# Kernel optimization log

Measured on AMD Instinct MI355X. Metric: run time of the kernel, lower is better.

The kernel has to match this reference:

```python
import jax, jax.numpy as jnp
import numpy as np

K = 32              # neighbors per node (loop=False in knn_graph)
NEG_SLOPE = 0.2     # GATv2Conv default negative_slope


def setup_inputs() -> dict:
    key = jax.random.key(0)
    ks = jax.random.split(key, 5)
    N, D_IN, D_OUT = 10000, 128, 256
    x = jax.random.normal(ks[0], (N, D_IN), dtype=jnp.float32)
    s_in = 1.0 / np.sqrt(D_IN)
    s_out = 1.0 / np.sqrt(D_OUT)
    return {
        "x": x,
        "W_l": jax.random.normal(ks[1], (D_IN, D_OUT), dtype=jnp.float32) * s_in,
        "b_l": jnp.zeros((D_OUT,), dtype=jnp.float32),
        "W_r": jax.random.normal(ks[2], (D_IN, D_OUT), dtype=jnp.float32) * s_in,
        "b_r": jnp.zeros((D_OUT,), dtype=jnp.float32),
        "att": jax.random.normal(ks[3], (D_OUT,), dtype=jnp.float32) * s_out,
        "bias": jnp.zeros((D_OUT,), dtype=jnp.float32),
    }


def _knn_indices(x, k):
    # Squared euclidean cdist, diagonal masked (loop=False), k smallest per row.
    sq = jnp.sum(x * x, axis=1)                       # [N]
    d = sq[:, None] + sq[None, :] - 2.0 * (x @ x.T)   # [N, N]
    d = d + jnp.diag(jnp.full((x.shape[0],), jnp.inf, dtype=x.dtype))
    _, nbr = jax.lax.top_k(-d, k)                     # [N, k] nearest neighbor ids
    return nbr


def reference(x, W_l, b_l, W_r, b_r, att, bias):
    N = x.shape[0]
    nbr = _knn_indices(x, K)                                   # [N, K]
    # GATv2Conv adds self-loops by default -> each node has K+1 sources.
    src = jnp.concatenate([nbr, jnp.arange(N)[:, None]], axis=1)  # [N, K+1]
    h_l = x @ W_l + b_l                                        # source transform [N, D]
    h_r = x @ W_r + b_r                                        # target transform [N, D]
    z = h_l[src] + h_r[:, None, :]                             # [N, K+1, D]
    e = jnp.einsum('nkd,d->nk', jax.nn.leaky_relu(z, NEG_SLOPE), att)  # [N, K+1]
    alpha = jax.nn.softmax(e, axis=1)                          # softmax over sources per target
    out = jnp.einsum('nk,nkd->nd', alpha, h_l[src]) + bias     # [N, D]
    return out
```

## Files before the change

### kernel.cpp

```cpp
#include <hip/hip_runtime.h>
#include <hip/hip_fp16.h>

#define NN     10000
#define DI     128
#define DO     256
#define KNB    32
#define NSRC   33
#define RB     16
#define NP2    10240
#define NTILE  640
#define ATILE  626
#define NCB    20
#define SEG    64
#define CAP    1024
#define RCAND  128
#define NEG    0.2f

typedef __attribute__((ext_vector_type(8))) short bf16x8;
typedef __attribute__((ext_vector_type(4))) float f32x4;

__device__ __forceinline__ unsigned fkey(float f) {
    unsigned u = __float_as_uint(f);
    return (u & 0x80000000u) ? ~u : (u | 0x80000000u);
}
__device__ __forceinline__ unsigned short bf16rne(float f) {
    unsigned u = __float_as_uint(f);
    unsigned r = u + 0x7FFFu + ((u >> 16) & 1u);
    return (unsigned short)(r >> 16);
}

__global__ __launch_bounds__(256) void prep_k(const float* __restrict__ x,
    unsigned short* __restrict__ Bh, double* __restrict__ sq64,
    float* __restrict__ sq32, unsigned* __restrict__ cnt)
{
    __shared__ float xs[16][132];
    const int t = threadIdx.x;
    const int tile = blockIdx.x;
    const int i0 = tile * 16;
    if (tile < 40) {
        const int idx = tile * 256 + t;
        if (idx < ATILE * 16) cnt[idx] = 0;
    }
#pragma unroll
    for (int q = 0; q < 2; ++q) {
        const int idx = t + 256 * q;
        const int r = idx >> 5, c4 = idx & 31;
        float4 v = make_float4(0.f, 0.f, 0.f, 0.f);
        if (i0 + r < NN) v = *(const float4*)(x + (size_t)(i0 + r) * DI + c4 * 4);
        *(float4*)&xs[r][c4 * 4] = v;
    }
    __syncthreads();
    const int ks = t >> 6, flane = t & 63;
    const int srow = flane & 15;
    const int kb = ks * 32 + ((flane >> 4) & 3) * 8;
    unsigned hi2[4];
#pragma unroll
    for (int j = 0; j < 4; ++j) {
        const float v0 = xs[srow][kb + 2 * j], v1 = xs[srow][kb + 2 * j + 1];
        hi2[j] = (unsigned)bf16rne(v0) | ((unsigned)bf16rne(v1) << 16);
    }
    *(uint4*)(Bh + ((size_t)(tile * 4 + ks) * 64 + flane) * 8) =
        make_uint4(hi2[0], hi2[1], hi2[2], hi2[3]);
    const int row = t >> 4, sub = t & 15;
    double s = 0.0;
#pragma unroll
    for (int q = 0; q < 8; ++q) {
        const float v = xs[row][sub * 8 + q];
        s = fma((double)v, (double)v, s);
    }
#pragma unroll
    for (int off = 8; off >= 1; off >>= 1) s += __shfl_xor(s, off);
    if (sub == 0) {
        const int gi = i0 + row;
        sq32[gi] = (gi < NN) ? (float)s : 0.f;
        if (gi < ATILE * 16) sq64[gi] = s;
    }
}

__global__ __launch_bounds__(256) void thresh_k(
    const unsigned short* __restrict__ Bh, const float* __restrict__ sq32,
    unsigned* __restrict__ Trow)
{
    __shared__ unsigned short dist16[RB][512];
    const int rt = blockIdx.x;
    const int r0 = rt * 16;
    const int t = threadIdx.x;
    const int wid = t >> 6, lane = t & 63;
    const int wbase = wid * 128, l15 = lane & 15, rgrp = (lane >> 4) * 4;

    bf16x8 ah[4];
#pragma unroll
    for (int ks = 0; ks < 4; ++ks)
        ah[ks] = *(const bf16x8*)(Bh + ((size_t)(rt * 4 + ks) * 64 + lane) * 8);
    float sqiv[4];
#pragma unroll
    for (int rg = 0; rg < 4; ++rg) sqiv[rg] = sq32[r0 + rgrp + rg];

#pragma unroll 1
    for (int ct = 0; ct < 8; ++ct) {
        const int ctg = wid * 8 + ct;
        bf16x8 bh[4];
#pragma unroll
        for (int ks = 0; ks < 4; ++ks)
            bh[ks] = *(const bf16x8*)(Bh + ((size_t)(ctg * 4 + ks) * 64 + lane) * 8);
        f32x4 acc = {0.f, 0.f, 0.f, 0.f};
#pragma unroll
        for (int ks = 0; ks < 4; ++ks)
            acc = __builtin_amdgcn_mfma_f32_16x16x32_bf16(ah[ks], bh[ks], acc, 0, 0, 0);
        const int col = wbase + ct * 16 + l15;
        const float sqj = sq32[col];
#pragma unroll
        for (int rg = 0; rg < 4; ++rg) {
            const int row = r0 + rgrp + rg;
            const float dd = __builtin_fmaf(-2.f, acc[rg], sqiv[rg] + sqj);
            unsigned k16 = (__float_as_uint(dd) >> 16) | 0x8000u;
            if (col >= NN || col == row) k16 = 0xFFFFu;
            dist16[rgrp + rg][col] = (unsigned short)k16;
        }
    }
    __syncthreads();

#pragma unroll 1
    for (int rr = 0; rr < 4; ++rr) {
        const int r = wid * 4 + rr;
        unsigned kk[8];
#pragma unroll
        for (int u = 0; u < 8; ++u) kk[u] = dist16[r][lane + 64 * u];
        unsigned lo = 0, hi = 0xFFFFu;
#pragma unroll 1
        for (int it = 0; it < 16; ++it) {
            const unsigned mid = (lo + hi) >> 1;
            int c2 = 0;
#pragma unroll
            for (int u = 0; u < 8; ++u)
                c2 += (int)__popcll(__ballot(kk[u] <= mid));
            if (c2 >= 16) hi = mid; else lo = mid;
        }
        if (lane == 0) Trow[r0 + r] = ((hi & 0x7FFFu) << 16) | 0xFFFFu;
    }
}

__global__ __launch_bounds__(256) void knn_emit_k(
    const unsigned short* __restrict__ Bh, const float* __restrict__ sq32,
    const unsigned* __restrict__ Trow, unsigned* __restrict__ cnt,
    unsigned* __restrict__ cand)
{
    __shared__ unsigned lcnt[32];
    __shared__ unsigned basebuf[32];
    __shared__ unsigned cbuf[32][SEG];
    const int r0 = blockIdx.x * 32;
    const int cbase = blockIdx.y * 512;
    const int t = threadIdx.x;
    const int wid = t >> 6, lane = t & 63;
    const int wbase = wid * 128, l15 = lane & 15, rgrp = (lane >> 4) * 4;
    if (t < 32) lcnt[t] = 0;

    bf16x8 ah[2][4];
#pragma unroll
    for (int rt2 = 0; rt2 < 2; ++rt2)
#pragma unroll
        for (int ks = 0; ks < 4; ++ks) {
            const int rt = (r0 >> 4) + rt2;
            ah[rt2][ks] = *(const bf16x8*)(Bh + ((size_t)(rt * 4 + ks) * 64 + lane) * 8);
        }
    float sqiv[2][4];
    unsigned TUv[2][4];
#pragma unroll
    for (int rt2 = 0; rt2 < 2; ++rt2)
#pragma unroll
        for (int rg = 0; rg < 4; ++rg) {
            const int row = r0 + rt2 * 16 + rgrp + rg;
            sqiv[rt2][rg] = sq32[row];
            TUv[rt2][rg] = Trow[row];
        }
    float sqjv[8];
#pragma unroll
    for (int ct = 0; ct < 8; ++ct)
        sqjv[ct] = sq32[cbase + wbase + ct * 16 + l15];
    __syncthreads();

    const int ctg0 = (cbase >> 4) + wid * 8;
    bf16x8 bh[4];
#pragma unroll
    for (int ks = 0; ks < 4; ++ks)
        bh[ks] = *(const bf16x8*)(Bh + ((size_t)(ctg0 * 4 + ks) * 64 + lane) * 8);

#pragma unroll 1
    for (int ct = 0; ct < 8; ++ct) {
        bf16x8 bhn[4];
        if (ct < 7) {
#pragma unroll
            for (int ks = 0; ks < 4; ++ks)
                bhn[ks] = *(const bf16x8*)(Bh + ((size_t)((ctg0 + ct + 1) * 4 + ks) * 64 + lane) * 8);
        }
        f32x4 a0 = {0.f, 0.f, 0.f, 0.f}, a1 = {0.f, 0.f, 0.f, 0.f};
#pragma unroll
        for (int ks = 0; ks < 4; ++ks) {
            a0 = __builtin_amdgcn_mfma_f32_16x16x32_bf16(ah[0][ks], bh[ks], a0, 0, 0, 0);
            a1 = __builtin_amdgcn_mfma_f32_16x16x32_bf16(ah[1][ks], bh[ks], a1, 0, 0, 0);
        }
        const int col = cbase + wbase + ct * 16 + l15;
        const float sqj = sqjv[ct];
#pragma unroll
        for (int rt2 = 0; rt2 < 2; ++rt2)
#pragma unroll
            for (int rg = 0; rg < 4; ++rg) {
                const int lrow = rt2 * 16 + rgrp + rg;
                const float dd = __builtin_fmaf(-2.f, (rt2 ? a1 : a0)[rg],
                                                sqiv[rt2][rg] + sqj);
                const unsigned raw = __float_as_uint(dd);
                if ((raw <= TUv[rt2][rg]) && (col < NN) && (col != r0 + lrow)) {
                    const unsigned slot = atomicAdd(&lcnt[lrow], 1u);
                    if (slot < SEG)
                        cbuf[lrow][slot] =
                            (((raw >> 16) | 0x8000u) << 16) | (unsigned)col;
                }
            }
#pragma unroll
        for (int ks = 0; ks < 4; ++ks) bh[ks] = bhn[ks];
    }

    __syncthreads();
    if (t < 32) {
        unsigned c = lcnt[t]; if (c > SEG) c = SEG;
        lcnt[t] = c;
        basebuf[t] = atomicAdd(&cnt[r0 + t], c);
    }
    __syncthreads();
#pragma unroll
    for (int q = 0; q < (32 * SEG) / 256; ++q) {
        const int idx = t + 256 * q;
        const int lr = idx >> 6, sl = idx & 63;
        if ((unsigned)sl < lcnt[lr]) {
            const unsigned b = basebuf[lr] + (unsigned)sl;
            if (b < CAP) cand[(size_t)(r0 + lr) * CAP + b] = cbuf[lr][sl];
        }
    }
}

__global__ __launch_bounds__(256) void rerank_select_k(
    const float* __restrict__ x, const double* __restrict__ sq64,
    const unsigned* __restrict__ cand, const unsigned* __restrict__ cnt,
    int* __restrict__ nbr)
{
    __shared__ unsigned hist[256];
    __shared__ unsigned hist2[256];
    __shared__ float xrs[DI];
    __shared__ unsigned cbuf[RCAND];
    __shared__ unsigned long long kbuf[RCAND];
    __shared__ unsigned sel[4];
    const int i = blockIdx.x, t = threadIdx.x;
    const int lane = t & 63;

    hist[t] = 0; hist2[t] = 0;
    if (t < RCAND) cbuf[t] = 0xFFFFFFFFu;
    if (t >= 128 && t < 160)
        *(float4*)&xrs[(t - 128) * 4] =
            *(const float4*)(x + (size_t)i * DI + (t - 128) * 4);
    if (t == 0) { sel[0] = 0xFFFFFFFFu; sel[2] = 0xFFFFu; sel[3] = 0; }
    unsigned n = cnt[i]; if (n > CAP) n = CAP;
    unsigned kk[4];
#pragma unroll
    for (int u = 0; u < 4; ++u) {
        const unsigned idx = (unsigned)t + 256u * u;
        kk[u] = (idx < n) ? cand[(size_t)i * CAP + idx] : 0xFFFFFFFFu;
    }
    __syncthreads();

#pragma unroll
    for (int u = 0; u < 4; ++u)
        if (kk[u] != 0xFFFFFFFFu) atomicAdd(&hist[kk[u] >> 24], 1u);
    __syncthreads();
    if (t < 64) {
        unsigned h[4];
#pragma unroll
        for (int q = 0; q < 4; ++q) h[q] = hist[lane * 4 + q];
        const unsigned s = h[0] + h[1] + h[2] + h[3];
        unsigned pre = s;
#pragma unroll
        for (int off = 1; off < 64; off <<= 1) {
            const unsigned o = __shfl_up(pre, off);
            if (lane >= off) pre += o;
        }
        const unsigned B = pre - s;
        if (B < 64 && B + s >= 64) {
            unsigned c = B, H = 0, rr = 0;
#pragma unroll
            for (int q = 0; q < 4; ++q) {
                if (c < 64 && c + h[q] >= 64) { H = lane * 4 + q; rr = 64 - c; break; }
                c += h[q];
            }
            sel[0] = H; sel[1] = rr;
        }
    }
    __syncthreads();
    const unsigned H = sel[0];

    if (H != 0xFFFFFFFFu) {
#pragma unroll
        for (int u = 0; u < 4; ++u)
            if (kk[u] != 0xFFFFFFFFu && (kk[u] >> 24) == H)
                atomicAdd(&hist2[(kk[u] >> 16) & 0xFFu], 1u);
    }
    __syncthreads();
    if (t < 64 && H != 0xFFFFFFFFu) {
        const unsigned r = sel[1];
        unsigned h[4];
#pragma unroll
        for (int q = 0; q < 4; ++q) h[q] = hist2[lane * 4 + q];
        const unsigned s = h[0] + h[1] + h[2] + h[3];
        unsigned pre = s;
#pragma unroll
        for (int off = 1; off < 64; off <<= 1) {
            const unsigned o = __shfl_up(pre, off);
            if (lane >= off) pre += o;
        }
        const unsigned B = pre - s;
        if (B < r && B + s >= r) {
            unsigned c = B, L = 0;
#pragma unroll
            for (int q = 0; q < 4; ++q) {
                if (c < r && c + h[q] >= r) { L = lane * 4 + q; break; }
                c += h[q];
            }
            sel[2] = (H << 8) | L;
        }
    }
    __syncthreads();
    const unsigned T16 = sel[2];

    {
        const unsigned long long lml = (1ull << lane) - 1;
#pragma unroll
        for (int u = 0; u < 4; ++u) {
            const bool pass = (kk[u] != 0xFFFFFFFFu) && ((kk[u] >> 16) <= T16);
            const unsigned long long b = __ballot(pass);
            unsigned base = 0;
            if (lane == 0 && b) base = atomicAdd(&sel[3], (unsigned)__popcll(b));
            base = __shfl(base, 0);
            if (pass) {
                const int slot = (int)(base + (unsigned)__popcll(b & lml));
                if (slot < RCAND) cbuf[slot] = kk[u];
            }
        }
    }
    __syncthreads();

    const int c = t >> 1, h = t & 1;
    const unsigned cc = cbuf[c];
    const int col = (int)(cc & 0xFFFFu);
    const bool valid = col < NN;
    const float* xc = x + (size_t)(valid ? col : 0) * DI;
    double a = 0.0;
#pragma unroll
    for (int q = 0; q < 16; ++q) {
        const int fi = q * 8 + h * 4;
        const float4 v = *(const float4*)(xc + fi);
        const float4 r4 = *(const float4*)(&xrs[fi]);
        a = fma((double)r4.x, (double)v.x, a);
        a = fma((double)r4.y, (double)v.y, a);
        a = fma((double)r4.z, (double)v.z, a);
        a = fma((double)r4.w, (double)v.w, a);
    }
    a += __shfl_xor(a, 1);
    if (h == 0) {
        unsigned long long key = ~0ull;
        if (valid) {
            const float dd = (float)(sq64[i] + sq64[col] - 2.0 * a);
            key = ((unsigned long long)fkey(dd) << 32) | (unsigned)col;
        }
        kbuf[c] = key;
    }
    __syncthreads();

    if (t < RCAND) {
        const unsigned long long key = kbuf[t];
        int rank = 0;
#pragma unroll 8
        for (int j = 0; j < RCAND; ++j)
            rank += (kbuf[j] < key) ? 1 : 0;
        if (key != ~0ull && rank < KNB)
            nbr[(size_t)i * KNB + rank] = (int)(key & 0xFFFFu);
    }
}

__global__ __launch_bounds__(256) void hgemm_k(
    const float* __restrict__ x, const float* __restrict__ Wl,
    const float* __restrict__ bl, const float* __restrict__ Wr,
    const float* __restrict__ br, __half* __restrict__ hl16, float* __restrict__ hr)
{
    const int c = threadIdx.x;
    const int r0 = blockIdx.x * RB;
    float accl[RB], accr[RB];
    const float blv = bl[c], brv = br[c];
#pragma unroll
    for (int r = 0; r < RB; ++r) { accl[r] = blv; accr[r] = brv; }
    for (int d = 0; d < DI; ++d) {
        const float wl = Wl[d * DO + c];
        const float wr = Wr[d * DO + c];
#pragma unroll
        for (int r = 0; r < RB; ++r) {
            const float xv = x[(size_t)(r0 + r) * DI + d];
            accl[r] = fmaf(xv, wl, accl[r]);
            accr[r] = fmaf(xv, wr, accr[r]);
        }
    }
#pragma unroll
    for (int r = 0; r < RB; ++r) {
        hl16[(size_t)(r0 + r) * DO + c] = __float2half(accl[r]);
        hr[(size_t)(r0 + r) * DO + c] = accr[r];
    }
}

__global__ __launch_bounds__(256) void gat_k(
    const __half* __restrict__ hl16, const float* __restrict__ hr,
    const int* __restrict__ nbr, const float* __restrict__ att,
    const float* __restrict__ bias, float* __restrict__ out)
{
    __shared__ int src[NSRC];
    __shared__ __align__(16) __half hbuf[NSRC][DO];
    __shared__ float eS[NSRC];
    __shared__ float alphaS[NSRC];
    const int i = blockIdx.x, t = threadIdx.x;
    if (t < KNB) src[t] = nbr[(size_t)i * KNB + t];
    if (t == KNB) src[KNB] = i;
    __syncthreads();

    {
        const int sub = t & 31, rb = t >> 5;
#pragma unroll
        for (int s = 0; s < 5; ++s) {
            const int rk = s * 8 + rb;
            if (rk < NSRC)
                *(uint4*)&hbuf[rk][sub * 8] =
                    *(const uint4*)(hl16 + (size_t)src[rk] * DO + sub * 8);
        }
    }
    __syncthreads();

    const int wid = t >> 6, lane = t & 63;
    {
        const float4 hr4 = *(const float4*)(hr + (size_t)i * DO + lane * 4);
        const float4 at4 = *(const float4*)(att + lane * 4);
#pragma unroll 1
        for (int k = wid; k < NSRC; k += 4) {
            const __half2 h01 = *(const __half2*)&hbuf[k][lane * 4];
            const __half2 h23 = *(const __half2*)&hbuf[k][lane * 4 + 2];
            const float2 f01 = __half22float2(h01);
            const float2 f23 = __half22float2(h23);
            float z, p = 0.f;
            z = f01.x + hr4.x; p = fmaf(z > 0.f ? z : NEG * z, at4.x, p);
            z = f01.y + hr4.y; p = fmaf(z > 0.f ? z : NEG * z, at4.y, p);
            z = f23.x + hr4.z; p = fmaf(z > 0.f ? z : NEG * z, at4.z, p);
            z = f23.y + hr4.w; p = fmaf(z > 0.f ? z : NEG * z, at4.w, p);
#pragma unroll
            for (int off = 32; off >= 1; off >>= 1) p += __shfl_xor(p, off);
            if (lane == 0) eS[k] = p;
        }
    }
    __syncthreads();
    if (wid == 0) {
        const float v = (lane < NSRC) ? eS[lane] : -3.4e38f;
        float m = v;
#pragma unroll
        for (int off = 32; off >= 1; off >>= 1) m = fmaxf(m, __shfl_xor(m, off));
        float w = (lane < NSRC) ? __expf(v - m) : 0.f;
        float s = w;
#pragma unroll
        for (int off = 32; off >= 1; off >>= 1) s += __shfl_xor(s, off);
        if (lane < NSRC) alphaS[lane] = w / s;
    }
    __syncthreads();
    float o = bias[t];
#pragma unroll
    for (int k = 0; k < NSRC; ++k)
        o = fmaf(alphaS[k], __half2float(hbuf[k][t]), o);
    out[(size_t)i * DO + t] = o;
}

extern "C" void kernel_launch(void* const* d_in, const int* in_sizes, int n_in,
                              void* d_out, int out_size, void* d_ws, size_t ws_size,
                              hipStream_t stream) {
    const float* x    = (const float*)d_in[0];
    const float* Wl   = (const float*)d_in[1];
    const float* bl   = (const float*)d_in[2];
    const float* Wr   = (const float*)d_in[3];
    const float* br   = (const float*)d_in[4];
    const float* att  = (const float*)d_in[5];
    const float* bias = (const float*)d_in[6];
    float* out = (float*)d_out;

    char* ws = (char*)d_ws;
    unsigned short* Bh  = (unsigned short*)(ws + 0);
    double* sq64 = (double*)(ws + 2621440);
    float*  sq32 = (float*)(ws + 2701568);
    unsigned* Trow = (unsigned*)(ws + 2742528);
    unsigned* cnt  = (unsigned*)(ws + 2782592);
    int*    nbr  = (int*)(ws + 2822656);
    unsigned* cand = (unsigned*)(ws + 4102656);
    __half* hl16 = (__half*)(ws + 4102656);
    float*  hr   = (float*)(ws + 9222656);

    prep_k<<<dim3(NTILE), 256, 0, stream>>>(x, Bh, sq64, sq32, cnt);
    thresh_k<<<dim3(ATILE), 256, 0, stream>>>(Bh, sq32, Trow);
    knn_emit_k<<<dim3(ATILE / 2, NCB), 256, 0, stream>>>(Bh, sq32, Trow, cnt, cand);
    rerank_select_k<<<dim3(NN), 256, 0, stream>>>(x, sq64, cand, cnt, nbr);
    hgemm_k<<<dim3(NN / RB), 256, 0, stream>>>(x, Wl, bl, Wr, br, hl16, hr);
    gat_k<<<dim3(NN), 256, 0, stream>>>(hl16, hr, nbr, att, bias, out);
}
```

Before: 235.4 us.

## Fuse feature GEMM into prep kernel and specialize KNN emit loop

```diff
diff --git a/kernel.cpp b/kernel.cpp
--- a/kernel.cpp
+++ b/kernel.cpp
@@ -31,7 +31,10 @@
 
 __global__ __launch_bounds__(256) void prep_k(const float* __restrict__ x,
     unsigned short* __restrict__ Bh, double* __restrict__ sq64,
-    float* __restrict__ sq32, unsigned* __restrict__ cnt)
+    float* __restrict__ sq32, unsigned* __restrict__ cnt,
+    const float* __restrict__ Wl, const float* __restrict__ bl,
+    const float* __restrict__ Wr, const float* __restrict__ br,
+    __half* __restrict__ hl16, float* __restrict__ hr)
 {
     __shared__ float xs[16][132];
     const int t = threadIdx.x;
@@ -50,30 +53,56 @@
         *(float4*)&xs[r][c4 * 4] = v;
     }
     __syncthreads();
-    const int ks = t >> 6, flane = t & 63;
-    const int srow = flane & 15;
-    const int kb = ks * 32 + ((flane >> 4) & 3) * 8;
-    unsigned hi2[4];
-#pragma unroll
-    for (int j = 0; j < 4; ++j) {
-        const float v0 = xs[srow][kb + 2 * j], v1 = xs[srow][kb + 2 * j + 1];
-        hi2[j] = (unsigned)bf16rne(v0) | ((unsigned)bf16rne(v1) << 16);
-    }
-    *(uint4*)(Bh + ((size_t)(tile * 4 + ks) * 64 + flane) * 8) =
-        make_uint4(hi2[0], hi2[1], hi2[2], hi2[3]);
-    const int row = t >> 4, sub = t & 15;
-    double s = 0.0;
-#pragma unroll
-    for (int q = 0; q < 8; ++q) {
-        const float v = xs[row][sub * 8 + q];
-        s = fma((double)v, (double)v, s);
-    }
-#pragma unroll
-    for (int off = 8; off >= 1; off >>= 1) s += __shfl_xor(s, off);
-    if (sub == 0) {
-        const int gi = i0 + row;
-        sq32[gi] = (gi < NN) ? (float)s : 0.f;
-        if (gi < ATILE * 16) sq64[gi] = s;
+    {
+        const int ks = t >> 6, flane = t & 63;
+        const int srow = flane & 15;
+        const int kb = ks * 32 + ((flane >> 4) & 3) * 8;
+        unsigned hi2[4];
+#pragma unroll
+        for (int j = 0; j < 4; ++j) {
+            const float v0 = xs[srow][kb + 2 * j], v1 = xs[srow][kb + 2 * j + 1];
+            hi2[j] = (unsigned)bf16rne(v0) | ((unsigned)bf16rne(v1) << 16);
+        }
+        *(uint4*)(Bh + ((size_t)(tile * 4 + ks) * 64 + flane) * 8) =
+            make_uint4(hi2[0], hi2[1], hi2[2], hi2[3]);
+    }
+    {
+        const int row = t >> 4, sub = t & 15;
+        double s = 0.0;
+#pragma unroll
+        for (int q = 0; q < 8; ++q) {
+            const float v = xs[row][sub * 8 + q];
+            s = fma((double)v, (double)v, s);
+        }
+#pragma unroll
+        for (int off = 8; off >= 1; off >>= 1) s += __shfl_xor(s, off);
+        if (sub == 0) {
+            const int gi = i0 + row;
+            sq32[gi] = (gi < NN) ? (float)s : 0.f;
+            if (gi < ATILE * 16) sq64[gi] = s;
+        }
+    }
+    if (tile < NN / RB) {
+        const int c = t;
+        float accl[RB], accr[RB];
+        const float blv = bl[c], brv = br[c];
+#pragma unroll
+        for (int r = 0; r < RB; ++r) { accl[r] = blv; accr[r] = brv; }
+        for (int d = 0; d < DI; ++d) {
+            const float wl = Wl[d * DO + c];
+            const float wr = Wr[d * DO + c];
+#pragma unroll
+            for (int r = 0; r < RB; ++r) {
+                const float xv = x[(size_t)(i0 + r) * DI + d];
+                accl[r] = fmaf(xv, wl, accl[r]);
+                accr[r] = fmaf(xv, wr, accr[r]);
+            }
+        }
+#pragma unroll
+        for (int r = 0; r < RB; ++r) {
+            hl16[(size_t)(i0 + r) * DO + c] = __float2half(accl[r]);
+            hr[(size_t)(i0 + r) * DO + c] = accr[r];
+        }
     }
 }
 
@@ -174,51 +203,69 @@
             TUv[rt2][rg] = Trow[row];
         }
     float sqjv[8];
-#pragma unroll
-    for (int ct = 0; ct < 8; ++ct)
-        sqjv[ct] = sq32[cbase + wbase + ct * 16 + l15];
+    unsigned colOr[8];
+#pragma unroll
+    for (int ct = 0; ct < 8; ++ct) {
+        const int col = cbase + wbase + ct * 16 + l15;
+        sqjv[ct] = sq32[col];
+        colOr[ct] = 0x80000000u | (unsigned)col;
+    }
     __syncthreads();
 
     const int ctg0 = (cbase >> 4) + wid * 8;
-    bf16x8 bh[4];
-#pragma unroll
-    for (int ks = 0; ks < 4; ++ks)
-        bh[ks] = *(const bf16x8*)(Bh + ((size_t)(ctg0 * 4 + ks) * 64 + lane) * 8);
-
-#pragma unroll 1
-    for (int ct = 0; ct < 8; ++ct) {
-        bf16x8 bhn[4];
-        if (ct < 7) {
-#pragma unroll
-            for (int ks = 0; ks < 4; ++ks)
-                bhn[ks] = *(const bf16x8*)(Bh + ((size_t)((ctg0 + ct + 1) * 4 + ks) * 64 + lane) * 8);
-        }
-        f32x4 a0 = {0.f, 0.f, 0.f, 0.f}, a1 = {0.f, 0.f, 0.f, 0.f};
-#pragma unroll
-        for (int ks = 0; ks < 4; ++ks) {
-            a0 = __builtin_amdgcn_mfma_f32_16x16x32_bf16(ah[0][ks], bh[ks], a0, 0, 0, 0);
-            a1 = __builtin_amdgcn_mfma_f32_16x16x32_bf16(ah[1][ks], bh[ks], a1, 0, 0, 0);
-        }
-        const int col = cbase + wbase + ct * 16 + l15;
-        const float sqj = sqjv[ct];
-#pragma unroll
-        for (int rt2 = 0; rt2 < 2; ++rt2)
-#pragma unroll
-            for (int rg = 0; rg < 4; ++rg) {
-                const int lrow = rt2 * 16 + rgrp + rg;
-                const float dd = __builtin_fmaf(-2.f, (rt2 ? a1 : a0)[rg],
-                                                sqiv[rt2][rg] + sqj);
-                const unsigned raw = __float_as_uint(dd);
-                if ((raw <= TUv[rt2][rg]) && (col < NN) && (col != r0 + lrow)) {
-                    const unsigned slot = atomicAdd(&lcnt[lrow], 1u);
-                    if (slot < SEG)
-                        cbuf[lrow][slot] =
-                            (((raw >> 16) | 0x8000u) << 16) | (unsigned)col;
-                }
-            }
-#pragma unroll
-        for (int ks = 0; ks < 4; ++ks) bh[ks] = bhn[ks];
-    }
+    const bool safe = ((blockIdx.x >> 4) != blockIdx.y) && (blockIdx.y != NCB - 1);
+
+#define LOADB(DST, CT) { \
+    _Pragma("unroll") \
+    for (int ks = 0; ks < 4; ++ks) \
+        DST[ks] = *(const bf16x8*)(Bh + ((size_t)((ctg0 + (CT)) * 4 + ks) * 64 + lane) * 8); }
+
+#define BODY(BHREG, CT, CHK) { \
+    f32x4 a0 = {0.f,0.f,0.f,0.f}, a1 = {0.f,0.f,0.f,0.f}; \
+    _Pragma("unroll") \
+    for (int ks = 0; ks < 4; ++ks) { \
+        a0 = __builtin_amdgcn_mfma_f32_16x16x32_bf16(ah[0][ks], BHREG[ks], a0, 0, 0, 0); \
+        a1 = __builtin_amdgcn_mfma_f32_16x16x32_bf16(ah[1][ks], BHREG[ks], a1, 0, 0, 0); } \
+    const float sqj = sqjv[CT]; \
+    const unsigned co = colOr[CT]; \
+    _Pragma("unroll") \
+    for (int rt2 = 0; rt2 < 2; ++rt2) \
+    _Pragma("unroll") \
+    for (int rg = 0; rg < 4; ++rg) { \
+        const int lrow = rt2 * 16 + rgrp + rg; \
+        const float dd = __builtin_fmaf(-2.f, (rt2 ? a1 : a0)[rg], sqiv[rt2][rg] + sqj); \
+        const unsigned raw = __float_as_uint(dd); \
+        bool pass = raw <= TUv[rt2][rg]; \
+        if (CHK) { \
+            const int col = (int)(co & 0xFFFFu); \
+            pass = pass && (col < NN) && (col != r0 + lrow); \
+        } \
+        if (pass) { \
+            const unsigned slot = atomicAdd(&lcnt[lrow], 1u); \
+            if (slot < SEG) cbuf[lrow][slot] = (raw & 0xFFFF0000u) | co; \
+        } } }
+
+    bf16x8 bA[4], bB[4];
+    LOADB(bA, 0)
+    if (safe) {
+#pragma unroll
+        for (int ct = 0; ct < 8; ct += 2) {
+            LOADB(bB, ct + 1)
+            BODY(bA, ct, false)
+            if (ct + 2 < 8) LOADB(bA, ct + 2)
+            BODY(bB, ct + 1, false)
+        }
+    } else {
+#pragma unroll
+        for (int ct = 0; ct < 8; ct += 2) {
+            LOADB(bB, ct + 1)
+            BODY(bA, ct, true)
+            if (ct + 2 < 8) LOADB(bA, ct + 2)
+            BODY(bB, ct + 1, true)
+        }
+    }
+#undef BODY
+#undef LOADB
 
     __syncthreads();
     if (t < 32) {
@@ -381,34 +428,6 @@
             rank += (kbuf[j] < key) ? 1 : 0;
         if (key != ~0ull && rank < KNB)
             nbr[(size_t)i * KNB + rank] = (int)(key & 0xFFFFu);
-    }
-}
-
-__global__ __launch_bounds__(256) void hgemm_k(
-    const float* __restrict__ x, const float* __restrict__ Wl,
-    const float* __restrict__ bl, const float* __restrict__ Wr,
-    const float* __restrict__ br, __half* __restrict__ hl16, float* __restrict__ hr)
-{
-    const int c = threadIdx.x;
-    const int r0 = blockIdx.x * RB;
-    float accl[RB], accr[RB];
-    const float blv = bl[c], brv = br[c];
-#pragma unroll
-    for (int r = 0; r < RB; ++r) { accl[r] = blv; accr[r] = brv; }
-    for (int d = 0; d < DI; ++d) {
-        const float wl = Wl[d * DO + c];
-        const float wr = Wr[d * DO + c];
-#pragma unroll
-        for (int r = 0; r < RB; ++r) {
-            const float xv = x[(size_t)(r0 + r) * DI + d];
-            accl[r] = fmaf(xv, wl, accl[r]);
-            accr[r] = fmaf(xv, wr, accr[r]);
-        }
-    }
-#pragma unroll
-    for (int r = 0; r < RB; ++r) {
-        hl16[(size_t)(r0 + r) * DO + c] = __float2half(accl[r]);
-        hr[(size_t)(r0 + r) * DO + c] = accr[r];
     }
 }
 
@@ -498,13 +517,13 @@
     unsigned* cnt  = (unsigned*)(ws + 2782592);
     int*    nbr  = (int*)(ws + 2822656);
     unsigned* cand = (unsigned*)(ws + 4102656);
-    __half* hl16 = (__half*)(ws + 4102656);
-    float*  hr   = (float*)(ws + 9222656);
-
-    prep_k<<<dim3(NTILE), 256, 0, stream>>>(x, Bh, sq64, sq32, cnt);
+    __half* hl16 = (__half*)(ws + 45128192);
+    float*  hr   = (float*)(ws + 50248192);
+
+    prep_k<<<dim3(NTILE), 256, 0, stream>>>(x, Bh, sq64, sq32, cnt,
+                                            Wl, bl, Wr, br, hl16, hr);
     thresh_k<<<dim3(ATILE), 256, 0, stream>>>(Bh, sq32, Trow);
     knn_emit_k<<<dim3(ATILE / 2, NCB), 256, 0, stream>>>(Bh, sq32, Trow, cnt, cand);
     rerank_select_k<<<dim3(NN), 256, 0, stream>>>(x, sq64, cand, cnt, nbr);
-    hgemm_k<<<dim3(NN / RB), 256, 0, stream>>>(x, Wl, bl, Wr, br, hl16, hr);
     gat_k<<<dim3(NN), 256, 0, stream>>>(hl16, hr, nbr, att, bias, out);
 }
```

Result: no change. 231.6 us (-1.6%).

## Fuse feature GEMM into prep and GAT attention into rerank kernel

Applied to the files above, without the earlier changes.

```diff
diff --git a/kernel.cpp b/kernel.cpp
--- a/kernel.cpp
+++ b/kernel.cpp
@@ -10,6 +10,7 @@
 #define NP2    10240
 #define NTILE  640
 #define ATILE  626
+#define NROWS  10016
 #define NCB    20
 #define SEG    64
 #define CAP    1024
@@ -31,7 +32,10 @@
 
 __global__ __launch_bounds__(256) void prep_k(const float* __restrict__ x,
     unsigned short* __restrict__ Bh, double* __restrict__ sq64,
-    float* __restrict__ sq32, unsigned* __restrict__ cnt)
+    float* __restrict__ sq32, unsigned* __restrict__ cnt,
+    const float* __restrict__ Wl, const float* __restrict__ bl,
+    const float* __restrict__ Wr, const float* __restrict__ br,
+    __half* __restrict__ hl16, float* __restrict__ hr)
 {
     __shared__ float xs[16][132];
     const int t = threadIdx.x;
@@ -39,7 +43,7 @@
     const int i0 = tile * 16;
     if (tile < 40) {
         const int idx = tile * 256 + t;
-        if (idx < ATILE * 16) cnt[idx] = 0;
+        if (idx < NROWS) cnt[idx] = 0;
     }
 #pragma unroll
     for (int q = 0; q < 2; ++q) {
@@ -50,30 +54,56 @@
         *(float4*)&xs[r][c4 * 4] = v;
     }
     __syncthreads();
-    const int ks = t >> 6, flane = t & 63;
-    const int srow = flane & 15;
-    const int kb = ks * 32 + ((flane >> 4) & 3) * 8;
-    unsigned hi2[4];
-#pragma unroll
-    for (int j = 0; j < 4; ++j) {
-        const float v0 = xs[srow][kb + 2 * j], v1 = xs[srow][kb + 2 * j + 1];
-        hi2[j] = (unsigned)bf16rne(v0) | ((unsigned)bf16rne(v1) << 16);
-    }
-    *(uint4*)(Bh + ((size_t)(tile * 4 + ks) * 64 + flane) * 8) =
-        make_uint4(hi2[0], hi2[1], hi2[2], hi2[3]);
-    const int row = t >> 4, sub = t & 15;
-    double s = 0.0;
-#pragma unroll
-    for (int q = 0; q < 8; ++q) {
-        const float v = xs[row][sub * 8 + q];
-        s = fma((double)v, (double)v, s);
-    }
-#pragma unroll
-    for (int off = 8; off >= 1; off >>= 1) s += __shfl_xor(s, off);
-    if (sub == 0) {
-        const int gi = i0 + row;
-        sq32[gi] = (gi < NN) ? (float)s : 0.f;
-        if (gi < ATILE * 16) sq64[gi] = s;
+    {
+        const int ks = t >> 6, flane = t & 63;
+        const int srow = flane & 15;
+        const int kb = ks * 32 + ((flane >> 4) & 3) * 8;
+        unsigned hi2[4];
+#pragma unroll
+        for (int j = 0; j < 4; ++j) {
+            const float v0 = xs[srow][kb + 2 * j], v1 = xs[srow][kb + 2 * j + 1];
+            hi2[j] = (unsigned)bf16rne(v0) | ((unsigned)bf16rne(v1) << 16);
+        }
+        *(uint4*)(Bh + ((size_t)(tile * 4 + ks) * 64 + flane) * 8) =
+            make_uint4(hi2[0], hi2[1], hi2[2], hi2[3]);
+    }
+    {
+        const int row = t >> 4, sub = t & 15;
+        double s = 0.0;
+#pragma unroll
+        for (int q = 0; q < 8; ++q) {
+            const float v = xs[row][sub * 8 + q];
+            s = fma((double)v, (double)v, s);
+        }
+#pragma unroll
+        for (int off = 8; off >= 1; off >>= 1) s += __shfl_xor(s, off);
+        if (sub == 0) {
+            const int gi = i0 + row;
+            sq32[gi] = (gi < NN) ? (float)s : 0.f;
+            if (gi < NROWS) sq64[gi] = s;
+        }
+    }
+    if (tile < NN / RB) {
+        const int c = t;
+        float accl[RB], accr[RB];
+        const float blv = bl[c], brv = br[c];
+#pragma unroll
+        for (int r = 0; r < RB; ++r) { accl[r] = blv; accr[r] = brv; }
+        for (int d = 0; d < DI; ++d) {
+            const float wl = Wl[d * DO + c];
+            const float wr = Wr[d * DO + c];
+#pragma unroll
+            for (int r = 0; r < RB; ++r) {
+                const float xv = x[(size_t)(i0 + r) * DI + d];
+                accl[r] = fmaf(xv, wl, accl[r]);
+                accr[r] = fmaf(xv, wr, accr[r]);
+            }
+        }
+#pragma unroll
+        for (int r = 0; r < RB; ++r) {
+            hl16[(size_t)(i0 + r) * DO + c] = __float2half(accl[r]);
+            hr[(size_t)(i0 + r) * DO + c] = accr[r];
+        }
     }
 }
 
@@ -180,19 +210,13 @@
     __syncthreads();
 
     const int ctg0 = (cbase >> 4) + wid * 8;
-    bf16x8 bh[4];
-#pragma unroll
-    for (int ks = 0; ks < 4; ++ks)
-        bh[ks] = *(const bf16x8*)(Bh + ((size_t)(ctg0 * 4 + ks) * 64 + lane) * 8);
 
 #pragma unroll 1
     for (int ct = 0; ct < 8; ++ct) {
-        bf16x8 bhn[4];
-        if (ct < 7) {
-#pragma unroll
-            for (int ks = 0; ks < 4; ++ks)
-                bhn[ks] = *(const bf16x8*)(Bh + ((size_t)((ctg0 + ct + 1) * 4 + ks) * 64 + lane) * 8);
-        }
+        bf16x8 bh[4];
+#pragma unroll
+        for (int ks = 0; ks < 4; ++ks)
+            bh[ks] = *(const bf16x8*)(Bh + ((size_t)((ctg0 + ct) * 4 + ks) * 64 + lane) * 8);
         f32x4 a0 = {0.f, 0.f, 0.f, 0.f}, a1 = {0.f, 0.f, 0.f, 0.f};
 #pragma unroll
         for (int ks = 0; ks < 4; ++ks) {
@@ -216,8 +240,6 @@
                             (((raw >> 16) | 0x8000u) << 16) | (unsigned)col;
                 }
             }
-#pragma unroll
-        for (int ks = 0; ks < 4; ++ks) bh[ks] = bhn[ks];
     }
 
     __syncthreads();
@@ -238,10 +260,12 @@
     }
 }
 
-__global__ __launch_bounds__(256) void rerank_select_k(
+__global__ __launch_bounds__(256) void rerank_gat_k(
     const float* __restrict__ x, const double* __restrict__ sq64,
     const unsigned* __restrict__ cand, const unsigned* __restrict__ cnt,
-    int* __restrict__ nbr)
+    const __half* __restrict__ hl16, const float* __restrict__ hr,
+    const float* __restrict__ att, const float* __restrict__ bias,
+    float* __restrict__ out)
 {
     __shared__ unsigned hist[256];
     __shared__ unsigned hist2[256];
@@ -249,6 +273,10 @@
     __shared__ unsigned cbuf[RCAND];
     __shared__ unsigned long long kbuf[RCAND];
     __shared__ unsigned sel[4];
+    __shared__ int srcS[NSRC];
+    __shared__ __align__(16) __half hbuf[NSRC][DO];
+    __shared__ float eS[NSRC];
+    __shared__ float alphaS[NSRC];
     const int i = blockIdx.x, t = threadIdx.x;
     const int lane = t & 63;
 
@@ -380,50 +408,9 @@
         for (int j = 0; j < RCAND; ++j)
             rank += (kbuf[j] < key) ? 1 : 0;
         if (key != ~0ull && rank < KNB)
-            nbr[(size_t)i * KNB + rank] = (int)(key & 0xFFFFu);
-    }
-}
-
-__global__ __launch_bounds__(256) void hgemm_k(
-    const float* __restrict__ x, const float* __restrict__ Wl,
-    const float* __restrict__ bl, const float* __restrict__ Wr,
-    const float* __restrict__ br, __half* __restrict__ hl16, float* __restrict__ hr)
-{
-    const int c = threadIdx.x;
-    const int r0 = blockIdx.x * RB;
-    float accl[RB], accr[RB];
-    const float blv = bl[c], brv = br[c];
-#pragma unroll
-    for (int r = 0; r < RB; ++r) { accl[r] = blv; accr[r] = brv; }
-    for (int d = 0; d < DI; ++d) {
-        const float wl = Wl[d * DO + c];
-        const float wr = Wr[d * DO + c];
-#pragma unroll
-        for (int r = 0; r < RB; ++r) {
-            const float xv = x[(size_t)(r0 + r) * DI + d];
-            accl[r] = fmaf(xv, wl, accl[r]);
-            accr[r] = fmaf(xv, wr, accr[r]);
-        }
-    }
-#pragma unroll
-    for (int r = 0; r < RB; ++r) {
-        hl16[(size_t)(r0 + r) * DO + c] = __float2half(accl[r]);
-        hr[(size_t)(r0 + r) * DO + c] = accr[r];
-    }
-}
-
-__global__ __launch_bounds__(256) void gat_k(
-    const __half* __restrict__ hl16, const float* __restrict__ hr,
-    const int* __restrict__ nbr, const float* __restrict__ att,
-    const float* __restrict__ bias, float* __restrict__ out)
-{
-    __shared__ int src[NSRC];
-    __shared__ __align__(16) __half hbuf[NSRC][DO];
-    __shared__ float eS[NSRC];
-    __shared__ float alphaS[NSRC];
-    const int i = blockIdx.x, t = threadIdx.x;
-    if (t < KNB) src[t] = nbr[(size_t)i * KNB + t];
-    if (t == KNB) src[KNB] = i;
+            srcS[rank] = (int)(key & 0xFFFFu);
+    }
+    if (t == 0) srcS[KNB] = i;
     __syncthreads();
 
     {
@@ -433,12 +420,12 @@
             const int rk = s * 8 + rb;
             if (rk < NSRC)
                 *(uint4*)&hbuf[rk][sub * 8] =
-                    *(const uint4*)(hl16 + (size_t)src[rk] * DO + sub * 8);
-        }
-    }
-    __syncthreads();
-
-    const int wid = t >> 6, lane = t & 63;
+                    *(const uint4*)(hl16 + (size_t)srcS[rk] * DO + sub * 8);
+        }
+    }
+    __syncthreads();
+
+    const int wid = t >> 6;
     {
         const float4 hr4 = *(const float4*)(hr + (size_t)i * DO + lane * 4);
         const float4 at4 = *(const float4*)(att + lane * 4);
@@ -496,15 +483,14 @@
     float*  sq32 = (float*)(ws + 2701568);
     unsigned* Trow = (unsigned*)(ws + 2742528);
     unsigned* cnt  = (unsigned*)(ws + 2782592);
-    int*    nbr  = (int*)(ws + 2822656);
-    unsigned* cand = (unsigned*)(ws + 4102656);
-    __half* hl16 = (__half*)(ws + 4102656);
-    float*  hr   = (float*)(ws + 9222656);
-
-    prep_k<<<dim3(NTILE), 256, 0, stream>>>(x, Bh, sq64, sq32, cnt);
+    unsigned* cand = (unsigned*)(ws + 2822656);
+    __half* hl16 = (__half*)(ws + 43848192);
+    float*  hr   = (float*)(ws + 48968192);
+
+    prep_k<<<dim3(NTILE), 256, 0, stream>>>(x, Bh, sq64, sq32, cnt,
+                                            Wl, bl, Wr, br, hl16, hr);
     thresh_k<<<dim3(ATILE), 256, 0, stream>>>(Bh, sq32, Trow);
     knn_emit_k<<<dim3(ATILE / 2, NCB), 256, 0, stream>>>(Bh, sq32, Trow, cnt, cand);
-    rerank_select_k<<<dim3(NN), 256, 0, stream>>>(x, sq64, cand, cnt, nbr);
-    hgemm_k<<<dim3(NN / RB), 256, 0, stream>>>(x, Wl, bl, Wr, br, hl16, hr);
-    gat_k<<<dim3(NN), 256, 0, stream>>>(hl16, hr, nbr, att, bias, out);
-}
+    rerank_gat_k<<<dim3(NN), 256, 0, stream>>>(x, sq64, cand, cnt,
+                                               hl16, hr, att, bias, out);
+}
```

New measurement: 230.4 us. 1.02x faster.
